# Optimization experiments

Measured on AMD Instinct MI355X. Metric: run time of the kernel, lower is better.

Reference implementation:

```python
import jax, jax.numpy as jnp
import numpy as np

DIM = 2048
N_HEADS = 16
N_KV_HEADS = 4
HEAD_DIM = 128
BASE = 1000.0
B, S = 2, 2048


def setup_inputs() -> dict:
    key = jax.random.key(0)
    ks = jax.random.split(key, 5)
    x = jax.random.normal(ks[0], (B, S, DIM), jnp.float32)
    scale = 1.0 / np.sqrt(DIM)
    Wq = jax.random.normal(ks[1], (DIM, N_HEADS * HEAD_DIM), jnp.float32) * scale
    Wk = jax.random.normal(ks[2], (DIM, N_KV_HEADS * HEAD_DIM), jnp.float32) * scale
    Wv = jax.random.normal(ks[3], (DIM, N_KV_HEADS * HEAD_DIM), jnp.float32) * scale
    Wo = jax.random.normal(ks[4], (N_HEADS * HEAD_DIM, DIM), jnp.float32) * scale
    mask = jnp.tril(jnp.ones((S, S), jnp.int32))  # causal mask from module-level constant
    return {"x": x, "Wq": Wq, "Wk": Wk, "Wv": Wv, "Wo": Wo, "mask": mask}


def _rope_tables(seq_len, head_dim, dtype):
    theta = 1.0 / BASE ** (jnp.arange(0, head_dim, 2, dtype=dtype) / head_dim)
    freqs = jnp.outer(jnp.arange(seq_len, dtype=dtype), theta)  # [S, D/2]
    # broadcast to [1, S, 1, D/2] over (batch, seq, heads, pairs)
    return jnp.cos(freqs)[None, :, None, :], jnp.sin(freqs)[None, :, None, :]


def _apply_rope(x, cos, sin):
    # interleaved RoPE: pairs (x[...,2i], x[...,2i+1])
    x1, x2 = x[..., ::2], x[..., 1::2]
    out = jnp.stack([x1 * cos - x2 * sin, x1 * sin + x2 * cos], axis=-1)
    return out.reshape(x.shape)


def reference(x, Wq, Wk, Wv, Wo, mask):
    batch, seq_len, _ = x.shape
    g = N_HEADS // N_KV_HEADS  # GQA repeat factor
    q = (x @ Wq).reshape(batch, seq_len, N_HEADS, HEAD_DIM)
    k = (x @ Wk).reshape(batch, seq_len, N_KV_HEADS, HEAD_DIM)
    v = (x @ Wv).reshape(batch, seq_len, N_KV_HEADS, HEAD_DIM)
    cos, sin = _rope_tables(seq_len, HEAD_DIM, x.dtype)
    q = _apply_rope(q, cos, sin)
    k = _apply_rope(k, cos, sin)
    # grouped-query attention without materializing repeated K/V:
    # q -> [b, s, kv, g, d]; scores -> [b, kv, g, q, kseq]
    q = q.reshape(batch, seq_len, N_KV_HEADS, g, HEAD_DIM)
    scale = HEAD_DIM ** -0.5
    scores = jnp.einsum("bqhgd,bkhd->bhgqk", q, k) * scale
    scores = jnp.where(mask == 0, float("-inf"), scores)
    attn = jax.nn.softmax(scores, axis=-1)
    out = jnp.einsum("bhgqk,bkhd->bqhgd", attn, v)
    out = out.reshape(batch, seq_len, N_HEADS * HEAD_DIM)
    return out @ Wo
```

## Files before the change

kernel.cpp:

```cpp
#include <hip/hip_runtime.h>
#include <hip/hip_bf16.h>

#define B_    2
#define S_    2048
#define DIM_  2048
#define H_    16
#define HKV_  4
#define D_    128
#define NQKV_ 3072
#define BS_   (B_*S_)

typedef __attribute__((ext_vector_type(8))) short short8;
typedef __attribute__((ext_vector_type(4))) float f32x4;

__device__ __forceinline__ unsigned short f2bf(float f) {
    union { float f; unsigned u; } v; v.f = f;
    unsigned r = (v.u + 0x7fffu + ((v.u >> 16) & 1u)) >> 16;
    return (unsigned short)r;
}
__device__ __forceinline__ float bf2f(unsigned short h) {
    union { unsigned u; float f; } v; v.u = ((unsigned)h) << 16;
    return v.f;
}

__global__ void k_convert(const float* __restrict__ in, unsigned short* __restrict__ out, int n4) {
    int i = blockIdx.x * blockDim.x + threadIdx.x;
    if (i >= n4) return;
    float4 v = ((const float4*)in)[i];
    union { unsigned short us[4]; unsigned long long u; } o;
    o.us[0] = f2bf(v.x); o.us[1] = f2bf(v.y); o.us[2] = f2bf(v.z); o.us[3] = f2bf(v.w);
    ((unsigned long long*)out)[i] = o.u;
}

__global__ void k_transpose(const float* __restrict__ W, unsigned short* __restrict__ WT,
                            int K, int N) {
    __shared__ float tile[64][65];
    const int k0 = blockIdx.x * 64, n0 = blockIdx.y * 64;
    const int tx = threadIdx.x & 63, ty = threadIdx.x >> 6;
    #pragma unroll
    for (int i = 0; i < 64; i += 4)
        tile[ty + i][tx] = W[(size_t)(k0 + ty + i) * N + n0 + tx];
    __syncthreads();
    #pragma unroll
    for (int i = 0; i < 64; i += 4)
        WT[(size_t)(n0 + ty + i) * K + k0 + tx] = f2bf(tile[tx][ty + i]);
}

template<typename OUT_T>
__global__ __launch_bounds__(256, 2)
void k_gemm_bt(const unsigned short* __restrict__ A,
               const unsigned short* __restrict__ BT,
               OUT_T* __restrict__ C, int M, int N, int K)
{
    __shared__ unsigned short lds_a[128 * 64];
    __shared__ unsigned short lds_b[128 * 64];
    const int tid  = threadIdx.x;
    const int nbn  = N >> 7;
    const int nwg  = gridDim.x;
    const int orig = blockIdx.x;
    const int q8   = nwg >> 3, r8 = nwg & 7;
    const int xcd  = orig & 7, lid = orig >> 3;
    const int wgid = (xcd < r8 ? xcd * (q8 + 1) : r8 * (q8 + 1) + (xcd - r8) * q8) + lid;
    const int bm   = wgid / nbn, bn = wgid % nbn;
    const int row0 = bm << 7, col0 = bn << 7;
    const int lane = tid & 63, wave = tid >> 6;
    const int wr = wave >> 1, wc = wave & 1;
    const int lg = lane >> 4, lr = lane & 15;

    f32x4 acc[4][4] = {};

    for (int kt = 0; kt < K; kt += 64) {
        __syncthreads();
        #pragma unroll
        for (int issue = 0; issue < 4; ++issue) {
            int e = issue * 2048 + wave * 512 + lane * 8;
            int r = e >> 6, kk = e & 63;
            const unsigned short* srcA = A  + (size_t)(row0 + r) * K + kt + kk;
            const unsigned short* srcB = BT + (size_t)(col0 + r) * K + kt + kk;
            unsigned short* dstA = lds_a + issue * 2048 + wave * 512;
            unsigned short* dstB = lds_b + issue * 2048 + wave * 512;
            __builtin_amdgcn_global_load_lds(
                (const __attribute__((address_space(1))) void*)srcA,
                (__attribute__((address_space(3))) void*)dstA, 16, 0, 0);
            __builtin_amdgcn_global_load_lds(
                (const __attribute__((address_space(1))) void*)srcB,
                (__attribute__((address_space(3))) void*)dstB, 16, 0, 0);
        }
        __syncthreads();
        #pragma unroll
        for (int kc = 0; kc < 2; ++kc) {
            short8 af[4], bf[4];
            #pragma unroll
            for (int m = 0; m < 4; ++m)
                af[m] = *(const short8*)&lds_a[(wr * 64 + m * 16 + lr) * 64 + kc * 32 + lg * 8];
            #pragma unroll
            for (int n = 0; n < 4; ++n)
                bf[n] = *(const short8*)&lds_b[(wc * 64 + n * 16 + lr) * 64 + kc * 32 + lg * 8];
            #pragma unroll
            for (int m = 0; m < 4; ++m)
                #pragma unroll
                for (int n = 0; n < 4; ++n)
                    acc[m][n] = __builtin_amdgcn_mfma_f32_16x16x32_bf16(af[m], bf[n], acc[m][n], 0, 0, 0);
        }
    }

    #pragma unroll
    for (int m = 0; m < 4; ++m)
        #pragma unroll
        for (int n = 0; n < 4; ++n)
            #pragma unroll
            for (int j = 0; j < 4; ++j) {
                int row = row0 + wr * 64 + m * 16 + lg * 4 + j;
                int col = col0 + wc * 64 + n * 16 + lr;
                if constexpr (sizeof(OUT_T) == 2)
                    C[(size_t)row * N + col] = (OUT_T)f2bf(acc[m][n][j]);
                else
                    C[(size_t)row * N + col] = (OUT_T)acc[m][n][j];
            }
}

__global__ void k_rope(unsigned short* __restrict__ qkv) {
    const int pair = blockIdx.x * 256 + threadIdx.x;
    const int row  = blockIdx.y;
    const int s    = row & (S_ - 1);
    const int col  = pair * 2;
    const int t    = (col & 127) >> 1;
    const float theta = exp2f(-((float)(2 * t) / 128.0f) * 9.965784284662087f);
    const float ang = (float)s * theta;
    const float sn = sinf(ang), cs = cosf(ang);
    unsigned short* p = qkv + (size_t)row * NQKV_ + col;
    float x1 = bf2f(p[0]), x2 = bf2f(p[1]);
    p[0] = f2bf(x1 * cs - x2 * sn);
    p[1] = f2bf(x1 * sn + x2 * cs);
}

__global__ void k_vtrans(const unsigned short* __restrict__ qkv, unsigned short* __restrict__ vt) {
    __shared__ unsigned short tile[64][65];
    const int s0 = blockIdx.x * 64;
    const int d0 = blockIdx.y * 64;
    const int bh = blockIdx.z;
    const int b = bh >> 2, hk = bh & 3;
    const int tx = threadIdx.x & 63, ty = threadIdx.x >> 6;
    #pragma unroll
    for (int i = 0; i < 64; i += 4)
        tile[i + ty][tx] = qkv[(size_t)(b * S_ + s0 + i + ty) * NQKV_ + (DIM_ + 512) + hk * D_ + d0 + tx];
    __syncthreads();
    #pragma unroll
    for (int i = 0; i < 64; i += 4)
        vt[((size_t)bh * D_ + d0 + i + ty) * S_ + s0 + tx] = tile[tx][i + ty];
}

#define KPAD 136
#define VPAD 72
#define SCALE2 0.12751739f

#define STAGE_LOAD(K0) do {                                                            \
    ks0 = *(const short8*)(kglob + (size_t)((K0) + (tid >> 4)) * NQKV_ + (tid & 15) * 8);      \
    ks1 = *(const short8*)(kglob + (size_t)((K0) + 32 + (tid >> 4)) * NQKV_ + (tid & 15) * 8); \
    vs0 = *(const short8*)(vglob + (size_t)(tid >> 3) * S_ + (K0) + (tid & 7) * 8);            \
    vs1 = *(const short8*)(vglob + (size_t)(64 + (tid >> 3)) * S_ + (K0) + (tid & 7) * 8);     \
} while (0)

#define ATTN_TILE(QF, QBASE, MYNT, TL, K0, HASNEXT, K0NEXT) do {                       \
    __syncthreads();                                                                   \
    *(short8*)&k_lds[(tid >> 4) * KPAD + (tid & 15) * 8] = ks0;                        \
    *(short8*)&k_lds[(32 + (tid >> 4)) * KPAD + (tid & 15) * 8] = ks1;                 \
    *(short8*)&v_lds[(tid >> 3) * VPAD + (tid & 7) * 8] = vs0;                         \
    *(short8*)&v_lds[(64 + (tid >> 3)) * VPAD + (tid & 7) * 8] = vs1;                  \
    __syncthreads();                                                                   \
    if (HASNEXT) { STAGE_LOAD(K0NEXT); }                                               \
    if ((TL) < (MYNT)) {                                                               \
        f32x4 sc[4];                                                                   \
        _Pragma("unroll")                                                              \
        for (int f = 0; f < 4; ++f) sc[f] = (f32x4){0.f, 0.f, 0.f, 0.f};               \
        _Pragma("unroll")                                                              \
        for (int f = 0; f < 4; ++f)                                                    \
            _Pragma("unroll")                                                          \
            for (int dc = 0; dc < 4; ++dc) {                                           \
                short8 kf = *(const short8*)&k_lds[(f * 16 + lr) * KPAD + dc * 32 + lg * 8]; \
                sc[f] = __builtin_amdgcn_mfma_f32_16x16x32_bf16(QF[dc], kf, sc[f], 0, 0, 0); \
            }                                                                          \
        _Pragma("unroll")                                                              \
        for (int f = 0; f < 4; ++f) {                                                  \
            int kpos = (K0) + f * 16 + lr;                                             \
            _Pragma("unroll")                                                          \
            for (int j = 0; j < 4; ++j) {                                              \
                int qpos = (QBASE) + lg * 4 + j;                                       \
                float s = sc[f][j] * SCALE2;                                           \
                sc[f][j] = (kpos <= qpos) ? s : -1e30f;                                \
            }                                                                          \
        }                                                                              \
        _Pragma("unroll")                                                              \
        for (int j = 0; j < 4; ++j) {                                                  \
            float mx = fmaxf(fmaxf(sc[0][j], sc[1][j]), fmaxf(sc[2][j], sc[3][j]));    \
            _Pragma("unroll")                                                          \
            for (int off = 1; off < 16; off <<= 1) mx = fmaxf(mx, __shfl_xor(mx, off));\
            float mnew = fmaxf(m_run[j], mx);                                          \
            float corr = exp2f(m_run[j] - mnew);                                       \
            float p0 = exp2f(sc[0][j] - mnew);                                         \
            float p1 = exp2f(sc[1][j] - mnew);                                         \
            float p2 = exp2f(sc[2][j] - mnew);                                         \
            float p3 = exp2f(sc[3][j] - mnew);                                         \
            float rs = (p0 + p1) + (p2 + p3);                                          \
            _Pragma("unroll")                                                          \
            for (int off = 1; off < 16; off <<= 1) rs += __shfl_xor(rs, off);          \
            l_run[j] = l_run[j] * corr + rs;                                           \
            m_run[j] = mnew;                                                           \
            _Pragma("unroll")                                                          \
            for (int c = 0; c < 8; ++c) oacc[c][j] *= corr;                            \
            int prow = (lg * 4 + j) * VPAD;                                            \
            p_my[prow + lr]      = f2bf(p0);                                           \
            p_my[prow + 16 + lr] = f2bf(p1);                                           \
            p_my[prow + 32 + lr] = f2bf(p2);                                           \
            p_my[prow + 48 + lr] = f2bf(p3);                                           \
        }                                                                              \
        asm volatile("s_waitcnt lgkmcnt(0)" ::: "memory");                             \
        _Pragma("unroll")                                                              \
        for (int kh = 0; kh < 2; ++kh) {                                               \
            short8 pf = *(const short8*)&p_my[lr * VPAD + kh * 32 + lg * 8];           \
            _Pragma("unroll")                                                          \
            for (int c = 0; c < 8; ++c) {                                              \
                short8 vf = *(const short8*)&v_lds[(c * 16 + lr) * VPAD + kh * 32 + lg * 8]; \
                oacc[c] = __builtin_amdgcn_mfma_f32_16x16x32_bf16(pf, vf, oacc[c], 0, 0, 0); \
            }                                                                          \
        }                                                                              \
    }                                                                                  \
} while (0)

__global__ __launch_bounds__(512, 2)
void k_attn(const unsigned short* __restrict__ qkv,
            const unsigned short* __restrict__ vt,
            unsigned short* __restrict__ o)
{
    __shared__ unsigned short k_lds[64 * KPAD];
    __shared__ unsigned short v_lds[128 * VPAD];
    __shared__ unsigned short p_lds[8 * 16 * VPAD];

    const int h = blockIdx.y, b = blockIdx.z;
    const int tid = threadIdx.x;
    const int lane = tid & 63, wave = tid >> 6;
    const int lg = lane >> 4, lr = lane & 15;
    const int hk = h >> 2;
    const int qlo = blockIdx.x, qhi = 15 - qlo;
    const int ntA = 2 * qlo + 2, ntB = 2 * qhi + 2;
    const int qbaseA = qlo * 128 + wave * 16;
    const int qbaseB = qhi * 128 + wave * 16;
    const int myA = ((qbaseA + 15) >> 6) + 1;
    const int myB = ((qbaseB + 15) >> 6) + 1;

    short8 qfA[4], qfB[4];
    {
        const unsigned short* qrA = qkv + (size_t)(b * S_ + qbaseA + lr) * NQKV_ + h * D_;
        const unsigned short* qrB = qkv + (size_t)(b * S_ + qbaseB + lr) * NQKV_ + h * D_;
        #pragma unroll
        for (int dc = 0; dc < 4; ++dc) {
            qfA[dc] = *(const short8*)(qrA + dc * 32 + lg * 8);
            qfB[dc] = *(const short8*)(qrB + dc * 32 + lg * 8);
        }
    }

    float m_run[4], l_run[4];
    #pragma unroll
    for (int j = 0; j < 4; ++j) { m_run[j] = -1e30f; l_run[j] = 0.f; }
    f32x4 oacc[8] = {};

    const unsigned short* kglob = qkv + (size_t)(b * S_) * NQKV_ + DIM_ + hk * D_;
    const unsigned short* vglob = vt + (size_t)(b * HKV_ + hk) * D_ * S_;
    unsigned short* p_my = p_lds + wave * 16 * VPAD;

    auto writeO = [&](int qb2) {
        #pragma unroll
        for (int j = 0; j < 4; ++j) {
            float inv = 1.0f / l_run[j];
            #pragma unroll
            for (int c = 0; c < 8; ++c)
                o[(size_t)(b * S_ + qb2 + lg * 4 + j) * DIM_ + h * D_ + c * 16 + lr] =
                    f2bf(oacc[c][j] * inv);
        }
    };

    short8 ks0, ks1, vs0, vs1;
    STAGE_LOAD(0);

    for (int t = 0; t < ntA; ++t) {
        int k0 = t * 64;
        int k0n = (t + 1 < ntA) ? (t + 1) * 64 : 0;
        ATTN_TILE(qfA, qbaseA, myA, t, k0, 1, k0n);
    }
    writeO(qbaseA);
    #pragma unroll
    for (int j = 0; j < 4; ++j) { m_run[j] = -1e30f; l_run[j] = 0.f; }
    #pragma unroll
    for (int c = 0; c < 8; ++c) oacc[c] = (f32x4){0.f, 0.f, 0.f, 0.f};

    for (int t = 0; t < ntB; ++t) {
        int k0 = t * 64;
        int k0n = (t + 1) * 64;
        ATTN_TILE(qfB, qbaseB, myB, t, k0, (t + 1 < ntB), k0n);
    }
    writeO(qbaseB);
}

extern "C" void kernel_launch(void* const* d_in, const int* in_sizes, int n_in,
                              void* d_out, int out_size, void* d_ws, size_t ws_size,
                              hipStream_t stream)
{
    const float* x  = (const float*)d_in[0];
    const float* Wq = (const float*)d_in[1];
    const float* Wk = (const float*)d_in[2];
    const float* Wv = (const float*)d_in[3];
    const float* Wo = (const float*)d_in[4];
    float* out = (float*)d_out;

    char* ws = (char*)d_ws;
    unsigned short* xb    = (unsigned short*)(ws);
    unsigned short* wqkvt = (unsigned short*)(ws + 16777216);
    unsigned short* wot   = (unsigned short*)(ws + 29360128);
    unsigned short* qkv   = (unsigned short*)(ws + 37748736);
    unsigned short* vt    = (unsigned short*)(ws + 62914560);
    unsigned short* attno = (unsigned short*)(ws + 67108864);

    k_convert<<<(BS_ * DIM_ / 4) / 256, 256, 0, stream>>>(x, xb, BS_ * DIM_ / 4);

    k_transpose<<<dim3(DIM_ / 64, DIM_ / 64), 256, 0, stream>>>(Wq, wqkvt, DIM_, 2048);
    k_transpose<<<dim3(DIM_ / 64, 512 / 64), 256, 0, stream>>>(Wk, wqkvt + (size_t)2048 * 2048, DIM_, 512);
    k_transpose<<<dim3(DIM_ / 64, 512 / 64), 256, 0, stream>>>(Wv, wqkvt + (size_t)2560 * 2048, DIM_, 512);
    k_transpose<<<dim3(DIM_ / 64, DIM_ / 64), 256, 0, stream>>>(Wo, wot, 2048, 2048);

    k_gemm_bt<unsigned short><<<(BS_ / 128) * (NQKV_ / 128), 256, 0, stream>>>(
        xb, wqkvt, qkv, BS_, NQKV_, DIM_);

    k_rope<<<dim3(5, BS_), 256, 0, stream>>>(qkv);

    k_vtrans<<<dim3(S_ / 64, D_ / 64, B_ * HKV_), 256, 0, stream>>>(qkv, vt);

    k_attn<<<dim3(8, H_, B_), 512, 0, stream>>>(qkv, vt, attno);

    k_gemm_bt<float><<<(BS_ / 128) * (DIM_ / 128), 256, 0, stream>>>(
        attno, wot, out, BS_, DIM_, DIM_);
}
```

Measured before the change: 375.8 us.

## Transpose attention MFMAs so softmax stays in registers and drop P LDS staging

Swaps the MFMA operand order so each lane holds one query row's scores across its accumulator registers. Row max and sum now need only two cross-lane shuffles instead of four per row, and running stats shrink to scalars. The probabilities are packed to bf16 and moved into the PV MFMA operand layout with __shfl instead of a round trip through LDS, which removes the P buffer and its lgkmcnt wait. The output store becomes 64-bit vectorized, in exchange for extra shuffle and select instructions per tile.

```diff
diff --git a/kernel.cpp b/kernel.cpp
--- a/kernel.cpp
+++ b/kernel.cpp
@@ -178,50 +178,61 @@
             _Pragma("unroll")                                                          \
             for (int dc = 0; dc < 4; ++dc) {                                           \
                 short8 kf = *(const short8*)&k_lds[(f * 16 + lr) * KPAD + dc * 32 + lg * 8]; \
-                sc[f] = __builtin_amdgcn_mfma_f32_16x16x32_bf16(QF[dc], kf, sc[f], 0, 0, 0); \
+                sc[f] = __builtin_amdgcn_mfma_f32_16x16x32_bf16(kf, QF[dc], sc[f], 0, 0, 0); \
             }                                                                          \
-        _Pragma("unroll")                                                              \
-        for (int f = 0; f < 4; ++f) {                                                  \
-            int kpos = (K0) + f * 16 + lr;                                             \
+        const int qpos = (QBASE) + lr;                                                 \
+        float mxl = -1e30f;                                                            \
+        _Pragma("unroll")                                                              \
+        for (int f = 0; f < 4; ++f)                                                    \
             _Pragma("unroll")                                                          \
             for (int j = 0; j < 4; ++j) {                                              \
-                int qpos = (QBASE) + lg * 4 + j;                                       \
+                int kpos = (K0) + f * 16 + lg * 4 + j;                                 \
                 float s = sc[f][j] * SCALE2;                                           \
                 sc[f][j] = (kpos <= qpos) ? s : -1e30f;                                \
+                mxl = fmaxf(mxl, sc[f][j]);                                            \
             }                                                                          \
+        mxl = fmaxf(mxl, __shfl_xor(mxl, 16));                                         \
+        mxl = fmaxf(mxl, __shfl_xor(mxl, 32));                                         \
+        float mnew = fmaxf(m_run, mxl);                                                \
+        float corr = exp2f(m_run - mnew);                                              \
+        m_run = mnew;                                                                  \
+        float rs = 0.f;                                                                \
+        _Pragma("unroll")                                                              \
+        for (int f = 0; f < 4; ++f)                                                    \
+            _Pragma("unroll")                                                          \
+            for (int j = 0; j < 4; ++j) {                                              \
+                sc[f][j] = exp2f(sc[f][j] - mnew);                                     \
+                rs += sc[f][j];                                                        \
+            }                                                                          \
+        rs += __shfl_xor(rs, 16);                                                      \
+        rs += __shfl_xor(rs, 32);                                                      \
+        l_run = l_run * corr + rs;                                                     \
+        _Pragma("unroll")                                                              \
+        for (int c = 0; c < 8; ++c)                                                    \
+            _Pragma("unroll")                                                          \
+            for (int j = 0; j < 4; ++j) oacc[c][j] *= corr;                            \
+        unsigned pk[4][2];                                                             \
+        _Pragma("unroll")                                                              \
+        for (int f = 0; f < 4; ++f) {                                                  \
+            pk[f][0] = (unsigned)f2bf(sc[f][0]) | ((unsigned)f2bf(sc[f][1]) << 16);    \
+            pk[f][1] = (unsigned)f2bf(sc[f][2]) | ((unsigned)f2bf(sc[f][3]) << 16);    \
         }                                                                              \
-        _Pragma("unroll")                                                              \
-        for (int j = 0; j < 4; ++j) {                                                  \
-            float mx = fmaxf(fmaxf(sc[0][j], sc[1][j]), fmaxf(sc[2][j], sc[3][j]));    \
-            _Pragma("unroll")                                                          \
-            for (int off = 1; off < 16; off <<= 1) mx = fmaxf(mx, __shfl_xor(mx, off));\
-            float mnew = fmaxf(m_run[j], mx);                                          \
-            float corr = exp2f(m_run[j] - mnew);                                       \
-            float p0 = exp2f(sc[0][j] - mnew);                                         \
-            float p1 = exp2f(sc[1][j] - mnew);                                         \
-            float p2 = exp2f(sc[2][j] - mnew);                                         \
-            float p3 = exp2f(sc[3][j] - mnew);                                         \
-            float rs = (p0 + p1) + (p2 + p3);                                          \
-            _Pragma("unroll")                                                          \
-            for (int off = 1; off < 16; off <<= 1) rs += __shfl_xor(rs, off);          \
-            l_run[j] = l_run[j] * corr + rs;                                           \
-            m_run[j] = mnew;                                                           \
-            _Pragma("unroll")                                                          \
-            for (int c = 0; c < 8; ++c) oacc[c][j] *= corr;                            \
-            int prow = (lg * 4 + j) * VPAD;                                            \
-            p_my[prow + lr]      = f2bf(p0);                                           \
-            p_my[prow + 16 + lr] = f2bf(p1);                                           \
-            p_my[prow + 32 + lr] = f2bf(p2);                                           \
-            p_my[prow + 48 + lr] = f2bf(p3);                                           \
-        }                                                                              \
-        asm volatile("s_waitcnt lgkmcnt(0)" ::: "memory");                             \
+        const int srcA = (lg & 1) * 32 + lr;                                           \
+        const int srcB = srcA + 16;                                                    \
+        const bool hiF = ((lg >> 1) != 0);                                             \
         _Pragma("unroll")                                                              \
         for (int kh = 0; kh < 2; ++kh) {                                               \
-            short8 pf = *(const short8*)&p_my[lr * VPAD + kh * 32 + lg * 8];           \
+            unsigned a0 = __shfl(pk[2 * kh][0], srcA), b0 = __shfl(pk[2 * kh + 1][0], srcA); \
+            unsigned a1 = __shfl(pk[2 * kh][1], srcA), b1 = __shfl(pk[2 * kh + 1][1], srcA); \
+            unsigned a2 = __shfl(pk[2 * kh][0], srcB), b2 = __shfl(pk[2 * kh + 1][0], srcB); \
+            unsigned a3 = __shfl(pk[2 * kh][1], srcB), b3 = __shfl(pk[2 * kh + 1][1], srcB); \
+            union { unsigned u[4]; short8 s8; } pf_;                                   \
+            pf_.u[0] = hiF ? b0 : a0; pf_.u[1] = hiF ? b1 : a1;                        \
+            pf_.u[2] = hiF ? b2 : a2; pf_.u[3] = hiF ? b3 : a3;                        \
             _Pragma("unroll")                                                          \
             for (int c = 0; c < 8; ++c) {                                              \
                 short8 vf = *(const short8*)&v_lds[(c * 16 + lr) * VPAD + kh * 32 + lg * 8]; \
-                oacc[c] = __builtin_amdgcn_mfma_f32_16x16x32_bf16(pf, vf, oacc[c], 0, 0, 0); \
+                oacc[c] = __builtin_amdgcn_mfma_f32_16x16x32_bf16(vf, pf_.s8, oacc[c], 0, 0, 0); \
             }                                                                          \
         }                                                                              \
     }                                                                                  \
@@ -234,7 +245,6 @@
 {
     __shared__ unsigned short k_lds[64 * KPAD];
     __shared__ unsigned short v_lds[128 * VPAD];
-    __shared__ unsigned short p_lds[8 * 16 * VPAD];
 
     const int h = blockIdx.y, b = blockIdx.z;
     const int tid = threadIdx.x;
@@ -259,23 +269,21 @@
         }
     }
 
-    float m_run[4], l_run[4];
-    #pragma unroll
-    for (int j = 0; j < 4; ++j) { m_run[j] = -1e30f; l_run[j] = 0.f; }
+    float m_run = -1e30f, l_run = 0.f;
     f32x4 oacc[8] = {};
 
     const unsigned short* kglob = qkv + (size_t)(b * S_) * NQKV_ + DIM_ + hk * D_;
     const unsigned short* vglob = vt + (size_t)(b * HKV_ + hk) * D_ * S_;
-    unsigned short* p_my = p_lds + wave * 16 * VPAD;
 
     auto writeO = [&](int qb2) {
-        #pragma unroll
-        for (int j = 0; j < 4; ++j) {
-            float inv = 1.0f / l_run[j];
-            #pragma unroll
-            for (int c = 0; c < 8; ++c)
-                o[(size_t)(b * S_ + qb2 + lg * 4 + j) * DIM_ + h * D_ + c * 16 + lr] =
-                    f2bf(oacc[c][j] * inv);
+        float inv = 1.0f / l_run;
+        unsigned short* orow = o + (size_t)(b * S_ + qb2 + lr) * DIM_ + h * D_ + lg * 4;
+        #pragma unroll
+        for (int c = 0; c < 8; ++c) {
+            union { unsigned short us[4]; unsigned long long u; } ov;
+            #pragma unroll
+            for (int j = 0; j < 4; ++j) ov.us[j] = f2bf(oacc[c][j] * inv);
+            *(unsigned long long*)(orow + c * 16) = ov.u;
         }
     };
 
@@ -288,8 +296,7 @@
         ATTN_TILE(qfA, qbaseA, myA, t, k0, 1, k0n);
     }
     writeO(qbaseA);
-    #pragma unroll
-    for (int j = 0; j < 4; ++j) { m_run[j] = -1e30f; l_run[j] = 0.f; }
+    m_run = -1e30f; l_run = 0.f;
     #pragma unroll
     for (int c = 0; c < 8; ++c) oacc[c] = (f32x4){0.f, 0.f, 0.f, 0.f};
 
```

Result: faster. 349.1 us (-7.1%).
